# Kernel tuning notes

Hardware: AMD Instinct MI355X
Metric: run time of the kernel (lower is better)

## Reference

```python
import jax, jax.numpy as jnp
import numpy as np


def log_g(x):
    # log of g(x) = where(x>=0, x+0.5, sigmoid(x)) in log space
    return jnp.where(x >= 0, jnp.log(jax.nn.relu(x) + 0.5), -jax.nn.softplus(-x))


def setup_inputs() -> dict:
    key = jax.random.key(0)
    k1, k2, k3 = jax.random.split(key, 3)
    B, S, D = 4, 4096, 2048
    D_INNER = int(D * 1.5)  # 3072
    x = jax.random.normal(k1, (B, S, D), dtype=jnp.float32)
    w_hg = jax.random.normal(k2, (D, 2 * D_INNER), dtype=jnp.float32) * (D ** -0.5)
    w_out = jax.random.normal(k3, (D_INNER, D), dtype=jnp.float32) * (D_INNER ** -0.5)
    return {"x": x, "w_hg": w_hg, "w_out": w_out}


def reference(x, w_hg, w_out):
    # x: [B,S,D]; w_hg: [D, 2*Di]; w_out: [Di, D]
    hg = jnp.einsum('bsd,de->bse', x, w_hg)
    hidden, gate = jnp.split(hg, 2, axis=-1)  # each [B,S,Di]
    log_coeffs = -jax.nn.softplus(gate)        # log(1 - z)
    log_z = -jax.nn.softplus(-gate)            # log z
    log_values = log_z + log_g(hidden)
    # Heinsen associative scan in log space along seq axis
    a_star = jnp.cumsum(log_coeffs, axis=1)
    log_h = a_star + jax.lax.cumlogsumexp(log_values - a_star, axis=1)
    h = jnp.exp(log_h)                         # [B,S,Di]
    out = jnp.einsum('bse,ed->bsd', h, w_out)  # to_out Linear (expansion != 1)
    return out
```

## Files before the change

kernel.cpp:

```cpp
#include <hip/hip_runtime.h>
#include <hip/hip_bf16.h>
#include <stdint.h>

typedef __hip_bfloat16 bf16;
typedef __attribute__((ext_vector_type(8))) short short8;
typedef __attribute__((ext_vector_type(4))) float floatx4;
typedef __attribute__((address_space(3))) const unsigned short lu16;

__device__ __forceinline__ unsigned short f2bu(float f) {
  bf16 b = __float2bfloat16(f);
  return *reinterpret_cast<unsigned short*>(&b);
}

__device__ __forceinline__ void stf(float* p, float v) { *p = v; }
__device__ __forceinline__ void stf(bf16* p, float v) { *p = __float2bfloat16(v); }

__device__ __forceinline__ void ld4(const bf16* p, float* o) {
  ushort4 v = *(const ushort4*)p;
  o[0] = __bfloat162float(*(bf16*)&v.x);
  o[1] = __bfloat162float(*(bf16*)&v.y);
  o[2] = __bfloat162float(*(bf16*)&v.z);
  o[3] = __bfloat162float(*(bf16*)&v.w);
}

__device__ __forceinline__ void gl_lds16(const bf16* g, bf16* l) {
  __builtin_amdgcn_global_load_lds((const __attribute__((address_space(1))) void*)g,
                                   (__attribute__((address_space(3))) void*)l,
                                   16, 0, 0);
}

template <int OFF>
__device__ __forceinline__ short8 ldsro(lu16* p) {
  short8 r;
  asm volatile("ds_read_b128 %0, %1 offset:%2" : "=v"(r) : "v"(p), "i"(OFF));
  return r;
}

#define BAR() __builtin_amdgcn_s_barrier()
#define WAITLG(n) do { asm volatile("s_waitcnt lgkmcnt(" #n ")" ::: "memory"); \
                       __builtin_amdgcn_sched_barrier(0); } while (0)
#define VMCNT(n) asm volatile("s_waitcnt vmcnt(" #n ")" ::: "memory")

__global__ void cvt_f32_bf16(const float* __restrict__ in, bf16* __restrict__ out, long n4) {
  long i = (long)blockIdx.x * blockDim.x + threadIdx.x;
  if (i >= n4) return;
  float4 v = ((const float4*)in)[i];
  ushort4 o;
  o.x = f2bu(v.x); o.y = f2bu(v.y); o.z = f2bu(v.z); o.w = f2bu(v.w);
  ((ushort4*)out)[i] = o;
}

__global__ void transpose_f32_to_bf16(const float* __restrict__ in, bf16* __restrict__ out,
                                      int R, int Cc) {
  __shared__ float tile[32][33];
  int tx = threadIdx.x & 31;
  int ty = threadIdx.x >> 5;
  int c0 = blockIdx.x * 32;
  int r0 = blockIdx.y * 32;
#pragma unroll
  for (int i = 0; i < 32; i += 8)
    tile[ty + i][tx] = in[(long)(r0 + ty + i) * Cc + c0 + tx];
  __syncthreads();
#pragma unroll
  for (int i = 0; i < 32; i += 8)
    out[(long)(c0 + ty + i) * R + r0 + tx] = __float2bfloat16(tile[tx][ty + i]);
}

template <typename OUT_T>
__global__ __launch_bounds__(512, 2) void gemm256(const bf16* __restrict__ A,
                                                  const bf16* __restrict__ BT,
                                                  OUT_T* __restrict__ C,
                                                  int M, int N, int K) {
  __shared__ __align__(16) bf16 lds[2][2][256][64];

  const int tid = threadIdx.x;
  const int w = tid >> 6;
  const int lane = tid & 63;
  const int quad = lane >> 4;
  const int r16 = lane & 15;
  const int wm = (w >> 2) * 128;
  const int wn = (w & 3) * 64;

  const int nbx = N >> 8;
  const int nwg = nbx * (M >> 8);
  const int bid = blockIdx.x;
  const int swz = (bid & 7) * (nwg >> 3) + (bid >> 3);
  const long bM = (long)(swz / nbx) * 256;
  const long bN = (long)(swz % nbx) * 256;

  const int r0 = tid >> 3;
  const int c8 = (tid & 7) ^ (r0 & 7);
  const bf16* Ag = A + (bM + r0) * (long)K + c8 * 8;
  const bf16* Bg = BT + (bN + r0) * (long)K + c8 * 8;
  const int lslot = w * 512;

  bf16* Am0 = &lds[0][0][0][0];
  bf16* Am1 = &lds[1][0][0][0];
  bf16* Bm0 = &lds[0][1][0][0];
  bf16* Bm1 = &lds[1][1][0][0];

  auto stage = [&](const bf16* g, bf16* lmat, int half, int kt) {
    const bf16* gs = g + (long)half * 128 * K + (long)kt * 64;
    bf16* ls = lmat + half * 8192 + lslot;
    gl_lds16(gs, ls);
    gl_lds16(gs + 64L * K, ls + 4096);
  };

  const int lofsA = (wm + r16) * 64;
  const int lofsB = (wn + r16) * 64;
  const int c8x0 = ((0 * 4 + quad) ^ (r16 & 7)) * 8;
  const int c8x1 = ((1 * 4 + quad) ^ (r16 & 7)) * 8;
  lu16* lb = (lu16*)&lds[0][0][0][0];
  lu16* pA0k0 = lb + 0 * 32768 + 0 * 16384 + lofsA + c8x0;
  lu16* pA0k1 = lb + 0 * 32768 + 0 * 16384 + lofsA + c8x1;
  lu16* pA1k0 = lb + 1 * 32768 + 0 * 16384 + lofsA + c8x0;
  lu16* pA1k1 = lb + 1 * 32768 + 0 * 16384 + lofsA + c8x1;
  lu16* pB0k0 = lb + 0 * 32768 + 1 * 16384 + lofsB + c8x0;
  lu16* pB0k1 = lb + 0 * 32768 + 1 * 16384 + lofsB + c8x1;
  lu16* pB1k0 = lb + 1 * 32768 + 1 * 16384 + lofsB + c8x0;
  lu16* pB1k1 = lb + 1 * 32768 + 1 * 16384 + lofsB + c8x1;

  floatx4 acc[8][4];
#pragma unroll
  for (int a = 0; a < 8; a++)
#pragma unroll
    for (int b = 0; b < 4; b++) acc[a][b] = (floatx4){0.f, 0.f, 0.f, 0.f};

  short8 af[4][2], bq0[2][2], bq1[2][2];

#define MMAG(AR, MF, NB, BQ) do { \
  acc[AR][NB]     = __builtin_amdgcn_mfma_f32_16x16x32_bf16(af[MF][0], BQ[0][0], acc[AR][NB], 0, 0, 0); \
  acc[AR][NB]     = __builtin_amdgcn_mfma_f32_16x16x32_bf16(af[MF][1], BQ[0][1], acc[AR][NB], 0, 0, 0); \
  acc[AR][NB + 1] = __builtin_amdgcn_mfma_f32_16x16x32_bf16(af[MF][0], BQ[1][0], acc[AR][NB + 1], 0, 0, 0); \
  acc[AR][NB + 1] = __builtin_amdgcn_mfma_f32_16x16x32_bf16(af[MF][1], BQ[1][1], acc[AR][NB + 1], 0, 0, 0); \
} while (0)

#define ISSUE_PA(PA0, PA1, PB0, PB1) do { \
  af[0][0] = ldsro<0>(PA0);     af[0][1] = ldsro<0>(PA1); \
  bq0[0][0] = ldsro<0>(PB0);    bq0[0][1] = ldsro<0>(PB1); \
  bq0[1][0] = ldsro<2048>(PB0); bq0[1][1] = ldsro<2048>(PB1); \
  af[1][0] = ldsro<2048>(PA0);  af[1][1] = ldsro<2048>(PA1); \
  af[2][0] = ldsro<4096>(PA0);  af[2][1] = ldsro<4096>(PA1); \
  af[3][0] = ldsro<6144>(PA0);  af[3][1] = ldsro<6144>(PA1); \
  bq1[0][0] = ldsro<4096>(PB0); bq1[0][1] = ldsro<4096>(PB1); \
  bq1[1][0] = ldsro<6144>(PB0); bq1[1][1] = ldsro<6144>(PB1); \
} while (0)

#define ISSUE_PB(PA0, PA1) do { \
  af[0][0] = ldsro<8192>(PA0);  af[0][1] = ldsro<8192>(PA1); \
  af[1][0] = ldsro<10240>(PA0); af[1][1] = ldsro<10240>(PA1); \
  af[2][0] = ldsro<12288>(PA0); af[2][1] = ldsro<12288>(PA1); \
  af[3][0] = ldsro<14336>(PA0); af[3][1] = ldsro<14336>(PA1); \
} while (0)

#define KTILE(PA0, PA1, PB0, PB1, SA1, SA2, SB1, SB2, VMX) do { \
   \
  ISSUE_PA(PA0, PA1, PB0, PB1); SA1; SA2; \
  __builtin_amdgcn_s_setprio(1); \
  WAITLG(10); MMAG(0, 0, 0, bq0); \
  WAITLG(8);  MMAG(1, 1, 0, bq0); \
  WAITLG(6);  MMAG(2, 2, 0, bq0); \
  WAITLG(4);  MMAG(3, 3, 0, bq0); \
  WAITLG(0); \
  MMAG(0, 0, 2, bq1); MMAG(1, 1, 2, bq1); MMAG(2, 2, 2, bq1); MMAG(3, 3, 2, bq1); \
  __builtin_amdgcn_s_setprio(0); BAR(); \
   \
  ISSUE_PB(PA0, PA1); SB1; SB2; \
  __builtin_amdgcn_s_setprio(1); \
  WAITLG(6); MMAG(4, 0, 0, bq0); MMAG(4, 0, 2, bq1); \
  WAITLG(4); MMAG(5, 1, 0, bq0); MMAG(5, 1, 2, bq1); \
  WAITLG(2); MMAG(6, 2, 0, bq0); MMAG(6, 2, 2, bq1); \
  WAITLG(0); MMAG(7, 3, 0, bq0); MMAG(7, 3, 2, bq1); \
  __builtin_amdgcn_s_setprio(0); \
  VMX; BAR(); \
} while (0)

  stage(Ag, Am0, 0, 0); stage(Ag, Am0, 1, 0);
  stage(Bg, Bm0, 0, 0); stage(Bg, Bm0, 1, 0);
  stage(Bg, Bm1, 0, 1); stage(Bg, Bm1, 1, 1);
  VMCNT(4);
  BAR();

  const int NI = K >> 7;
  for (int i = 0; i < NI - 1; ++i) {
    const int k1 = 2 * i + 1, k2 = 2 * i + 2, k3 = 2 * i + 3;
    KTILE(pA0k0, pA0k1, pB0k0, pB0k1,
          stage(Ag, Am1, 0, k1), stage(Ag, Am1, 1, k1),
          stage(Bg, Bm0, 0, k2), stage(Bg, Bm0, 1, k2), VMCNT(4));
    KTILE(pA1k0, pA1k1, pB1k0, pB1k1,
          stage(Ag, Am0, 0, k2), stage(Ag, Am0, 1, k2),
          stage(Bg, Bm1, 0, k3), stage(Bg, Bm1, 1, k3), VMCNT(4));
  }
  {
    const int kl = 2 * NI - 1;
    KTILE(pA0k0, pA0k1, pB0k0, pB0k1,
          stage(Ag, Am1, 0, kl), stage(Ag, Am1, 1, kl),
          (void)0, (void)0, VMCNT(0));
    KTILE(pA1k0, pA1k1, pB1k0, pB1k1,
          (void)0, (void)0, (void)0, (void)0, (void)0);
  }

#undef KTILE
#undef ISSUE_PB
#undef ISSUE_PA
#undef MMAG

#pragma unroll
  for (int mf = 0; mf < 8; ++mf) {
#pragma unroll
    for (int i2 = 0; i2 < 4; ++i2) {
      long row = bM + wm + mf * 16 + quad * 4 + i2;
      OUT_T* crow = C + row * (long)N + bN + wn + r16;
#pragma unroll
      for (int nf = 0; nf < 4; ++nf) stf(&crow[nf * 16], acc[mf][nf][i2]);
    }
  }
}

__device__ __forceinline__ void cv_compute(float hval, float gval, float& c, float& v) {
  float eg = __expf(gval);
  c = 1.f / (1.f + eg);
  float z = 1.f - c;
  float gx = (hval >= 0.f) ? (hval + 0.5f) : (1.f / (1.f + __expf(-hval)));
  v = z * gx;
}

__global__ void scan_pass1(const bf16* __restrict__ hg, float* __restrict__ P,
                           float* __restrict__ V, int S, int Di, int NN, int nch) {
  int tid = blockIdx.x * blockDim.x + threadIdx.x;
  int De = Di >> 2;
  int e = (tid % De) * 4;
  int rest = tid / De;
  int ch = rest % nch;
  int b = rest / nch;
  int CH = S / nch;
  const bf16* ph = hg + ((long)(b * S + ch * CH)) * NN + e;
  float Pv[4] = {1.f, 1.f, 1.f, 1.f}, Vv[4] = {0.f, 0.f, 0.f, 0.f};
  for (int t = 0; t < CH; t++) {
    float hv[4], gv[4];
    ld4(ph, hv);
    ld4(ph + Di, gv);
#pragma unroll
    for (int j = 0; j < 4; j++) {
      float c, v;
      cv_compute(hv[j], gv[j], c, v);
      Pv[j] *= c;
      Vv[j] = fmaf(c, Vv[j], v);
    }
    ph += NN;
  }
  long base = ((long)(b * nch + ch)) * Di + e;
  *(float4*)&P[base] = make_float4(Pv[0], Pv[1], Pv[2], Pv[3]);
  *(float4*)&V[base] = make_float4(Vv[0], Vv[1], Vv[2], Vv[3]);
}

__global__ void scan_pass2(const float* __restrict__ P, const float* __restrict__ V,
                           float* __restrict__ Hc, int Di, int nch) {
  int tid = blockIdx.x * blockDim.x + threadIdx.x;
  int e = tid % Di;
  int b = tid / Di;
  float H = 0.f;
  for (int j = 0; j < nch; j++) {
    long idx = ((long)(b * nch + j)) * Di + e;
    Hc[idx] = H;
    H = fmaf(P[idx], H, V[idx]);
  }
}

__global__ void scan_pass3(const bf16* __restrict__ hg, const float* __restrict__ Hc,
                           bf16* __restrict__ h, int S, int Di, int NN, int nch) {
  int tid = blockIdx.x * blockDim.x + threadIdx.x;
  int De = Di >> 2;
  int e = (tid % De) * 4;
  int rest = tid / De;
  int ch = rest % nch;
  int b = rest / nch;
  int CH = S / nch;
  const bf16* ph = hg + ((long)(b * S + ch * CH)) * NN + e;
  bf16* po = h + ((long)(b * S + ch * CH)) * Di + e;
  long base = ((long)(b * nch + ch)) * Di + e;
  float4 hc = *(const float4*)&Hc[base];
  float H[4] = {hc.x, hc.y, hc.z, hc.w};
  for (int t = 0; t < CH; t++) {
    float hv[4], gv[4];
    ld4(ph, hv);
    ld4(ph + Di, gv);
    ushort4 o;
#pragma unroll
    for (int j = 0; j < 4; j++) {
      float c, v;
      cv_compute(hv[j], gv[j], c, v);
      H[j] = fmaf(c, H[j], v);
    }
    o.x = f2bu(H[0]); o.y = f2bu(H[1]); o.z = f2bu(H[2]); o.w = f2bu(H[3]);
    *(ushort4*)po = o;
    ph += NN;
    po += Di;
  }
}

extern "C" void kernel_launch(void* const* d_in, const int* in_sizes, int n_in,
                              void* d_out, int out_size, void* d_ws, size_t ws_size,
                              hipStream_t stream) {
  const int B = 4, S = 4096, D = 2048, Di = 3072, NN = 6144;
  const int Mr = B * S;
  const int NCH = 64;

  const float* x = (const float*)d_in[0];
  const float* w_hg = (const float*)d_in[1];
  const float* w_out = (const float*)d_in[2];
  float* out = (float*)d_out;

  char* wp = (char*)d_ws;
  bf16* x_bf = (bf16*)wp;  wp += (size_t)Mr * D * 2;
  bf16* whgT = (bf16*)wp;  wp += (size_t)NN * D * 2;
  bf16* woutT = (bf16*)wp; wp += (size_t)D * Di * 2;
  bf16* h_bf = (bf16*)wp;  wp += (size_t)Mr * Di * 2;
  bf16* hg = (bf16*)wp;    wp += (size_t)Mr * NN * 2;

  float* P = (float*)x_bf;
  float* V = P + (size_t)B * NCH * Di;
  float* Hc = V + (size_t)B * NCH * Di;

  cvt_f32_bf16<<<(int)(((long)Mr * D / 4 + 255) / 256), 256, 0, stream>>>(x, x_bf, (long)Mr * D / 4);
  transpose_f32_to_bf16<<<dim3(NN / 32, D / 32), 256, 0, stream>>>(w_hg, whgT, D, NN);
  transpose_f32_to_bf16<<<dim3(D / 32, Di / 32), 256, 0, stream>>>(w_out, woutT, Di, D);

  const int nwg1 = (NN / 256) * (Mr / 256);
  const int nwg2 = (D / 256) * (Mr / 256);
  int scan_vthreads = B * NCH * (Di / 4);

  gemm256<bf16><<<nwg1, 512, 0, stream>>>(x_bf, whgT, hg, Mr, NN, D);
  scan_pass1<<<scan_vthreads / 256, 256, 0, stream>>>(hg, P, V, S, Di, NN, NCH);
  scan_pass2<<<(B * Di) / 256, 256, 0, stream>>>(P, V, Hc, Di, NCH);
  scan_pass3<<<scan_vthreads / 256, 256, 0, stream>>>(hg, Hc, h_bf, S, Di, NN, NCH);

  gemm256<float><<<nwg2, 512, 0, stream>>>(h_bf, woutT, out, Mr, D, Di);
}
```

Before: 930.3 us.

## Switch GEMM inner loop from 16x16x32 to 32x32x16 bf16 MFMA tiles

Replaces the 16x16x32 MFMA micro-tiling with 32x32x16 MFMA instructions. Each wave now holds a 4x2 grid of 32x32 accumulators, and the LDS fragment addressing, swizzle and wait-count schedule are rewritten to match. The aim is fewer MFMA issues and fewer LDS fragment loads per unit of work, since the larger instruction gives more reuse per operand. The risk is that the new XOR swizzle causes LDS bank conflicts, that the reworked epilogue writes less coalesced output, or that the waitcnt values are mismatched.

```diff
diff --git a/kernel.cpp b/kernel.cpp
--- a/kernel.cpp
+++ b/kernel.cpp
@@ -4,8 +4,9 @@
 
 typedef __hip_bfloat16 bf16;
 typedef __attribute__((ext_vector_type(8))) short short8;
-typedef __attribute__((ext_vector_type(4))) float floatx4;
+typedef __attribute__((ext_vector_type(16))) float floatx16;
 typedef __attribute__((address_space(3))) const unsigned short lu16;
+typedef __attribute__((address_space(3))) const char lchar;
 
 __device__ __forceinline__ unsigned short f2bu(float f) {
   bf16 b = __float2bfloat16(f);
@@ -76,8 +77,6 @@
   const int tid = threadIdx.x;
   const int w = tid >> 6;
   const int lane = tid & 63;
-  const int quad = lane >> 4;
-  const int r16 = lane & 15;
   const int wm = (w >> 2) * 128;
   const int wn = (w & 3) * 64;
 
@@ -106,71 +105,65 @@
     gl_lds16(gs + 64L * K, ls + 4096);
   };
 
-  const int lofsA = (wm + r16) * 64;
-  const int lofsB = (wn + r16) * 64;
-  const int c8x0 = ((0 * 4 + quad) ^ (r16 & 7)) * 8;
-  const int c8x1 = ((1 * 4 + quad) ^ (r16 & 7)) * 8;
-  lu16* lb = (lu16*)&lds[0][0][0][0];
-  lu16* pA0k0 = lb + 0 * 32768 + 0 * 16384 + lofsA + c8x0;
-  lu16* pA0k1 = lb + 0 * 32768 + 0 * 16384 + lofsA + c8x1;
-  lu16* pA1k0 = lb + 1 * 32768 + 0 * 16384 + lofsA + c8x0;
-  lu16* pA1k1 = lb + 1 * 32768 + 0 * 16384 + lofsA + c8x1;
-  lu16* pB0k0 = lb + 0 * 32768 + 1 * 16384 + lofsB + c8x0;
-  lu16* pB0k1 = lb + 0 * 32768 + 1 * 16384 + lofsB + c8x1;
-  lu16* pB1k0 = lb + 1 * 32768 + 1 * 16384 + lofsB + c8x0;
-  lu16* pB1k1 = lb + 1 * 32768 + 1 * 16384 + lofsB + c8x1;
-
-  floatx4 acc[8][4];
-#pragma unroll
-  for (int a = 0; a < 8; a++)
-#pragma unroll
-    for (int b = 0; b < 4; b++) acc[a][b] = (floatx4){0.f, 0.f, 0.f, 0.f};
-
-  short8 af[4][2], bq0[2][2], bq1[2][2];
-
-#define MMAG(AR, MF, NB, BQ) do { \
-  acc[AR][NB]     = __builtin_amdgcn_mfma_f32_16x16x32_bf16(af[MF][0], BQ[0][0], acc[AR][NB], 0, 0, 0); \
-  acc[AR][NB]     = __builtin_amdgcn_mfma_f32_16x16x32_bf16(af[MF][1], BQ[0][1], acc[AR][NB], 0, 0, 0); \
-  acc[AR][NB + 1] = __builtin_amdgcn_mfma_f32_16x16x32_bf16(af[MF][0], BQ[1][0], acc[AR][NB + 1], 0, 0, 0); \
-  acc[AR][NB + 1] = __builtin_amdgcn_mfma_f32_16x16x32_bf16(af[MF][1], BQ[1][1], acc[AR][NB + 1], 0, 0, 0); \
+  const int l31 = lane & 31, l7 = lane & 7, hi5 = lane >> 5;
+  const int aA = (wm + l31) * 128 + ((hi5 ^ l7) * 16);
+  const int aB = (wn + l31) * 128 + ((hi5 ^ l7) * 16);
+  lchar* lb8 = (lchar*)&lds[0][0][0][0];
+
+#define PTA(BUF, T) ((lu16*)(lb8 + (((aA) ^ ((T) * 32)) + (BUF) * 65536)))
+#define PTB(BUF, T) ((lu16*)(lb8 + (((aB) ^ ((T) * 32)) + 32768 + (BUF) * 65536)))
+
+  floatx16 acc[4][2];
+#pragma unroll
+  for (int a = 0; a < 4; a++)
+#pragma unroll
+    for (int b = 0; b < 2; b++)
+#pragma unroll
+      for (int i = 0; i < 16; i++) acc[a][b][i] = 0.f;
+
+  short8 af[4][2], bf[2][4];
+
+#define MMA4(NB, TA, TB) do { \
+  acc[0][NB] = __builtin_amdgcn_mfma_f32_32x32x16_bf16(af[0][TA], bf[NB][TB], acc[0][NB], 0, 0, 0); \
+  acc[1][NB] = __builtin_amdgcn_mfma_f32_32x32x16_bf16(af[1][TA], bf[NB][TB], acc[1][NB], 0, 0, 0); \
+  acc[2][NB] = __builtin_amdgcn_mfma_f32_32x32x16_bf16(af[2][TA], bf[NB][TB], acc[2][NB], 0, 0, 0); \
+  acc[3][NB] = __builtin_amdgcn_mfma_f32_32x32x16_bf16(af[3][TA], bf[NB][TB], acc[3][NB], 0, 0, 0); \
 } while (0)
 
-#define ISSUE_PA(PA0, PA1, PB0, PB1) do { \
-  af[0][0] = ldsro<0>(PA0);     af[0][1] = ldsro<0>(PA1); \
-  bq0[0][0] = ldsro<0>(PB0);    bq0[0][1] = ldsro<0>(PB1); \
-  bq0[1][0] = ldsro<2048>(PB0); bq0[1][1] = ldsro<2048>(PB1); \
-  af[1][0] = ldsro<2048>(PA0);  af[1][1] = ldsro<2048>(PA1); \
-  af[2][0] = ldsro<4096>(PA0);  af[2][1] = ldsro<4096>(PA1); \
-  af[3][0] = ldsro<6144>(PA0);  af[3][1] = ldsro<6144>(PA1); \
-  bq1[0][0] = ldsro<4096>(PB0); bq1[0][1] = ldsro<4096>(PB1); \
-  bq1[1][0] = ldsro<6144>(PB0); bq1[1][1] = ldsro<6144>(PB1); \
+#define ISSUE_PA(BUF) do { \
+  lu16 *pa0 = PTA(BUF, 0), *pb0 = PTB(BUF, 0), *pa1 = PTA(BUF, 1), *pb1 = PTB(BUF, 1); \
+  lu16 *pb2 = PTB(BUF, 2), *pb3 = PTB(BUF, 3); \
+  af[0][0] = ldsro<0>(pa0); af[1][0] = ldsro<4096>(pa0); \
+  af[2][0] = ldsro<8192>(pa0); af[3][0] = ldsro<12288>(pa0); \
+  bf[0][0] = ldsro<0>(pb0); bf[1][0] = ldsro<4096>(pb0); \
+  af[0][1] = ldsro<0>(pa1); af[1][1] = ldsro<4096>(pa1); \
+  af[2][1] = ldsro<8192>(pa1); af[3][1] = ldsro<12288>(pa1); \
+  bf[0][1] = ldsro<0>(pb1); bf[1][1] = ldsro<4096>(pb1); \
+  bf[0][2] = ldsro<0>(pb2); bf[1][2] = ldsro<4096>(pb2); \
+  bf[0][3] = ldsro<0>(pb3); bf[1][3] = ldsro<4096>(pb3); \
 } while (0)
 
-#define ISSUE_PB(PA0, PA1) do { \
-  af[0][0] = ldsro<8192>(PA0);  af[0][1] = ldsro<8192>(PA1); \
-  af[1][0] = ldsro<10240>(PA0); af[1][1] = ldsro<10240>(PA1); \
-  af[2][0] = ldsro<12288>(PA0); af[2][1] = ldsro<12288>(PA1); \
-  af[3][0] = ldsro<14336>(PA0); af[3][1] = ldsro<14336>(PA1); \
+#define ISSUE_PB(BUF) do { \
+  lu16 *pa2 = PTA(BUF, 2), *pa3 = PTA(BUF, 3); \
+  af[0][0] = ldsro<0>(pa2); af[1][0] = ldsro<4096>(pa2); \
+  af[2][0] = ldsro<8192>(pa2); af[3][0] = ldsro<12288>(pa2); \
+  af[0][1] = ldsro<0>(pa3); af[1][1] = ldsro<4096>(pa3); \
+  af[2][1] = ldsro<8192>(pa3); af[3][1] = ldsro<12288>(pa3); \
 } while (0)
 
-#define KTILE(PA0, PA1, PB0, PB1, SA1, SA2, SB1, SB2, VMX) do { \
-   \
-  ISSUE_PA(PA0, PA1, PB0, PB1); SA1; SA2; \
+#define KTILE(BUF, SA1, SA2, SB1, SB2, VMX) do { \
+  ISSUE_PA(BUF); SA1; SA2; \
   __builtin_amdgcn_s_setprio(1); \
-  WAITLG(10); MMAG(0, 0, 0, bq0); \
-  WAITLG(8);  MMAG(1, 1, 0, bq0); \
-  WAITLG(6);  MMAG(2, 2, 0, bq0); \
-  WAITLG(4);  MMAG(3, 3, 0, bq0); \
+  WAITLG(11); MMA4(0, 0, 0); \
+  WAITLG(10); MMA4(1, 0, 0); \
+  WAITLG(5);  MMA4(0, 1, 1); \
+  WAITLG(4);  MMA4(1, 1, 1); \
   WAITLG(0); \
-  MMAG(0, 0, 2, bq1); MMAG(1, 1, 2, bq1); MMAG(2, 2, 2, bq1); MMAG(3, 3, 2, bq1); \
   __builtin_amdgcn_s_setprio(0); BAR(); \
-   \
-  ISSUE_PB(PA0, PA1); SB1; SB2; \
+  ISSUE_PB(BUF); SB1; SB2; \
   __builtin_amdgcn_s_setprio(1); \
-  WAITLG(6); MMAG(4, 0, 0, bq0); MMAG(4, 0, 2, bq1); \
-  WAITLG(4); MMAG(5, 1, 0, bq0); MMAG(5, 1, 2, bq1); \
-  WAITLG(2); MMAG(6, 2, 0, bq0); MMAG(6, 2, 2, bq1); \
-  WAITLG(0); MMAG(7, 3, 0, bq0); MMAG(7, 3, 2, bq1); \
+  WAITLG(4); MMA4(0, 0, 2); MMA4(1, 0, 2); \
+  WAITLG(0); MMA4(0, 1, 3); MMA4(1, 1, 3); \
   __builtin_amdgcn_s_setprio(0); \
   VMX; BAR(); \
 } while (0)
@@ -184,35 +177,40 @@
   const int NI = K >> 7;
   for (int i = 0; i < NI - 1; ++i) {
     const int k1 = 2 * i + 1, k2 = 2 * i + 2, k3 = 2 * i + 3;
-    KTILE(pA0k0, pA0k1, pB0k0, pB0k1,
+    KTILE(0,
           stage(Ag, Am1, 0, k1), stage(Ag, Am1, 1, k1),
           stage(Bg, Bm0, 0, k2), stage(Bg, Bm0, 1, k2), VMCNT(4));
-    KTILE(pA1k0, pA1k1, pB1k0, pB1k1,
+    KTILE(1,
           stage(Ag, Am0, 0, k2), stage(Ag, Am0, 1, k2),
           stage(Bg, Bm1, 0, k3), stage(Bg, Bm1, 1, k3), VMCNT(4));
   }
   {
     const int kl = 2 * NI - 1;
-    KTILE(pA0k0, pA0k1, pB0k0, pB0k1,
+    KTILE(0,
           stage(Ag, Am1, 0, kl), stage(Ag, Am1, 1, kl),
           (void)0, (void)0, VMCNT(0));
-    KTILE(pA1k0, pA1k1, pB1k0, pB1k1,
+    KTILE(1,
           (void)0, (void)0, (void)0, (void)0, (void)0);
   }
 
 #undef KTILE
 #undef ISSUE_PB
 #undef ISSUE_PA
-#undef MMAG
-
-#pragma unroll
-  for (int mf = 0; mf < 8; ++mf) {
-#pragma unroll
-    for (int i2 = 0; i2 < 4; ++i2) {
-      long row = bM + wm + mf * 16 + quad * 4 + i2;
-      OUT_T* crow = C + row * (long)N + bN + wn + r16;
-#pragma unroll
-      for (int nf = 0; nf < 4; ++nf) stf(&crow[nf * 16], acc[mf][nf][i2]);
+#undef MMA4
+#undef PTB
+#undef PTA
+
+#pragma unroll
+  for (int mb = 0; mb < 4; ++mb) {
+#pragma unroll
+    for (int q = 0; q < 4; ++q) {
+#pragma unroll
+      for (int r2 = 0; r2 < 4; ++r2) {
+        long row = bM + wm + mb * 32 + q * 8 + r2 + 4 * hi5;
+        OUT_T* crow = C + row * (long)N + bN + wn + l31;
+        stf(&crow[0],  acc[mb][0][q * 4 + r2]);
+        stf(&crow[32], acc[mb][1][q * 4 + r2]);
+      }
     }
   }
 }
```

After: 981.1 us. +5.5%, slower.
